# Kernel optimization log

Measured on AMD Instinct MI355X. Metric: run time of the kernel, lower is better.

The kernel has to match this reference:

```python
import jax, jax.numpy as jnp
import numpy as np

NEG = 1e12  # matches the torch code's -1e12 '-inf' substitute


def setup_inputs() -> dict:
    key = jax.random.key(0)
    k1, k2, k3, k4 = jax.random.split(key, 4)
    B, L, H, O = 8, 512, 768, 12
    inputs = jax.random.normal(k1, (B, L, H), dtype=jnp.float32)
    mask = jax.random.randint(k2, (B, L), 0, 2, dtype=jnp.int32)
    # kaiming-uniform-ish init scale
    bound1 = 1.0 / np.sqrt(H)
    weight1 = jax.random.uniform(k3, (H, O, H), dtype=jnp.float32, minval=-bound1, maxval=bound1)
    bound2 = 1.0 / np.sqrt(2 * H + 1)
    weight2 = jax.random.uniform(k4, (2 * H + 1, O), dtype=jnp.float32, minval=-bound2, maxval=bound2)
    return {"inputs": inputs, "weight1": weight1, "weight2": weight2, "mask": mask}


def reference(inputs, weight1, weight2, mask):
    B, L, H = inputs.shape
    # bilinear term: bxyo = x_i W1 x_j
    logits1 = jnp.einsum('bxi,ioj,byj->bxyo', inputs, weight1, inputs)
    # linear term: equivalent to cat([x_i, x_j, 1]) @ weight2, without the O(L^2*H) intermediate.
    # concat_x[b,i,j] = [inputs[b,i], inputs[b,j], 1]
    wa = weight2[:H]          # multiplies x_i (the x2/row side)
    wb = weight2[H:2 * H]     # multiplies x_j (the x1/col side)
    bias = weight2[2 * H]     # multiplies the ones column
    lin_i = inputs @ wa       # [B, L, O]
    lin_j = inputs @ wb       # [B, L, O]
    logits = logits1 + lin_i[:, :, None, :] + lin_j[:, None, :, :] + bias
    logits = jnp.transpose(logits, (0, 3, 1, 2))  # [B, O, L, L]
    m = mask.astype(logits.dtype)
    m_row = m[:, None, :, None]  # mask on axis ndim-2
    m_col = m[:, None, None, :]  # mask on axis ndim-1
    logits = logits * m_row - NEG * (1.0 - m_row)
    logits = logits * m_col - NEG * (1.0 - m_col)
    tril = jnp.tril(jnp.ones((L, L), logits.dtype), k=-1)
    logits = logits - tril * NEG
    return logits
```

## Files before the change

kernel.cpp:

```cpp
#include <hip/hip_runtime.h>


#define NEGV 1e12f

typedef __attribute__((ext_vector_type(4))) float f32x4;
typedef __attribute__((ext_vector_type(8))) int   i32x8;

__device__ __forceinline__ unsigned char f2fp8(float f) {
    union { float f; unsigned u; } c; c.f = f;
    unsigned s = (c.u >> 24) & 0x80;
    unsigned a = c.u & 0x7FFFFFFF;
    if (a < 0x3C800000u) return (unsigned char)s;
    a += 0x80000;
    int e = (int)(a >> 23) - 127;
    unsigned m = (a >> 20) & 7;
    if (e > 8 || (e == 8 && m == 7)) return (unsigned char)(s | 0x7E);
    return (unsigned char)(s | ((e + 7) << 3) | m);
}

__device__ __forceinline__ unsigned pk_fp8x2(float a, float b) {
#if __has_builtin(__builtin_amdgcn_cvt_pk_fp8_f32)
    return (unsigned)__builtin_amdgcn_cvt_pk_fp8_f32(a, b, 0, false) & 0xFFFFu;
#else
    return (unsigned)f2fp8(a) | ((unsigned)f2fp8(b) << 8);
#endif
}

__device__ __forceinline__ float fp8_to_f32(unsigned char b) {
#if __has_builtin(__builtin_amdgcn_cvt_f32_fp8)
    return __builtin_amdgcn_cvt_f32_fp8((int)b, 0);
#else
    const int s = b >> 7, e = (b >> 3) & 15, m = b & 7;
    float mag = e ? __builtin_ldexpf((float)(8 + m), e - 10)
                  : __builtin_ldexpf((float)m, -9);
    return s ? -mag : mag;
#endif
}

#define GLDS(gp, lp) __builtin_amdgcn_global_load_lds( \
    (__attribute__((address_space(1))) void*)(gp),     \
    (__attribute__((address_space(3))) void*)(lp), 16, 0, 0)

__global__ __launch_bounds__(256) void prep_kernel(
    const float* __restrict__ in, const float* __restrict__ w1,
    const float* __restrict__ w2, unsigned* __restrict__ A8,
    unsigned char* __restrict__ W8) {
    __shared__ float t[64][68];
    const int bx  = blockIdx.x;
    const int tid = threadIdx.x;
    if (bx < 3072) {
        const int i = bx * 256 + tid;
        float4 v = ((const float4*)in)[i];
        A8[i] = pk_fp8x2(v.x, v.y) | (pk_fp8x2(v.z, v.w) << 16);
    } else if (bx < 4800) {
        const int b2 = bx - 3072;
        const int n0 = (b2 % 144) * 64;
        const int i0 = (b2 / 144) * 64;
        const int g  = tid >> 4;
        const int q  = tid & 15;
        #pragma unroll
        for (int p = 0; p < 4; ++p) {
            const int il = p * 16 + g;
            float4 v = *(const float4*)(w1 + (size_t)(i0 + il) * 9216 + n0 + q * 4);
            *(float4*)&t[il][q * 4] = v;
        }
        __syncthreads();
        #pragma unroll
        for (int p = 0; p < 4; ++p) {
            const int nl = p * 16 + g;
            const int iq = q * 4;
            const unsigned lo = pk_fp8x2(t[iq    ][nl] * 16.0f, t[iq + 1][nl] * 16.0f);
            const unsigned hi = pk_fp8x2(t[iq + 2][nl] * 16.0f, t[iq + 3][nl] * 16.0f);
            *(unsigned*)(W8 + (size_t)(n0 + nl) * 768 + i0 + iq) = lo | (hi << 16);
        }
    } else {
        const int j = bx - 4800;
        unsigned char* dst = W8 + (size_t)(9216 + j) * 768;
        if (j < 24) {
            #pragma unroll
            for (int k = 0; k < 3; ++k) {
                const int h = tid * 3 + k;
                const int col = (j < 12) ? (h * 12 + j) : ((768 + h) * 12 + (j - 12));
                dst[h] = (unsigned char)(pk_fp8x2(w2[col] * 16.0f, 0.0f) & 0xFF);
            }
        } else {
            if (tid < 192) ((unsigned*)dst)[tid] = 0u;
        }
    }
}

template <bool COUNTED>
__device__ __forceinline__ void gemm256_fp8(
    const unsigned char* __restrict__ A, int lda,
    const unsigned char* __restrict__ B, int ldb,
    char* As, char* Bs, f32x4 (&acc)[8][4], int sA, int sB) {
    const int tid  = threadIdx.x;
    const int lane = tid & 63;
    const int wave = tid >> 6;
    const unsigned char* aSrc[4]; const unsigned char* bSrc[4];
    int off[4];
    #pragma unroll
    for (int p = 0; p < 4; ++p) {
        const int cc = tid + 512 * p;
        const int row = cc >> 3, slot = cc & 7;
        const int g = slot ^ (row & 7);
        aSrc[p] = A + (size_t)row * lda + g * 16;
        bSrc[p] = B + (size_t)row * ldb + g * 16;
        off[p] = cc * 16;
    }
    const int wm = (wave >> 2) * 128;
    const int wn = (wave & 3) * 64;
    const int fr = lane & 15;
    const int kg = lane >> 4;

    if (!COUNTED) {
        #pragma unroll
        for (int p = 0; p < 4; ++p) GLDS(aSrc[p], As + off[p]);
        #pragma unroll
        for (int p = 0; p < 4; ++p) GLDS(bSrc[p], Bs + off[p]);
        __syncthreads();
        int cur = 0;
        for (int t = 1; t <= 6; ++t) {
            const int nxt = cur ^ 1;
            if (t < 6) {
                const int kk = t * 128;
                #pragma unroll
                for (int p = 0; p < 4; ++p) GLDS(aSrc[p] + kk, As + nxt * 32768 + off[p]);
                #pragma unroll
                for (int p = 0; p < 4; ++p) GLDS(bSrc[p] + kk, Bs + nxt * 32768 + off[p]);
            }
            const char* Ab = As + cur * 32768;
            const char* Bb = Bs + cur * 32768;
            i32x8 bf[4];
            #pragma unroll
            for (int ni = 0; ni < 4; ++ni) {
                const int r = wn + ni * 16 + fr;
                const uint4 lo = *(const uint4*)(Bb + r * 128 + ((2 * kg    ) ^ (r & 7)) * 16);
                const uint4 hi = *(const uint4*)(Bb + r * 128 + ((2 * kg + 1) ^ (r & 7)) * 16);
                bf[ni][0] = lo.x; bf[ni][1] = lo.y; bf[ni][2] = lo.z; bf[ni][3] = lo.w;
                bf[ni][4] = hi.x; bf[ni][5] = hi.y; bf[ni][6] = hi.z; bf[ni][7] = hi.w;
            }
            #pragma unroll
            for (int mi = 0; mi < 8; ++mi) {
                const int r = wm + mi * 16 + fr;
                const uint4 lo = *(const uint4*)(Ab + r * 128 + ((2 * kg    ) ^ (r & 7)) * 16);
                const uint4 hi = *(const uint4*)(Ab + r * 128 + ((2 * kg + 1) ^ (r & 7)) * 16);
                i32x8 af;
                af[0] = lo.x; af[1] = lo.y; af[2] = lo.z; af[3] = lo.w;
                af[4] = hi.x; af[5] = hi.y; af[6] = hi.z; af[7] = hi.w;
                #pragma unroll
                for (int ni = 0; ni < 4; ++ni)
                    acc[mi][ni] = __builtin_amdgcn_mfma_scale_f32_16x16x128_f8f6f4(
                        af, bf[ni], acc[mi][ni], 0, 0, 0, sA, 0, sB);
            }
            __syncthreads();
            cur = nxt;
        }
        return;
    }

    #pragma unroll
    for (int p = 0; p < 4; ++p) GLDS(aSrc[p], As + off[p]);
    #pragma unroll
    for (int p = 0; p < 4; ++p) GLDS(bSrc[p], Bs + off[p]);
    #pragma unroll
    for (int p = 0; p < 4; ++p) GLDS(aSrc[p] + 128, As + 32768 + off[p]);
    #pragma unroll
    for (int p = 0; p < 4; ++p) GLDS(bSrc[p] + 128, Bs + 32768 + off[p]);

    #pragma unroll
    for (int t = 0; t < 6; ++t) {
        const int cur = t & 1;
        if (t < 5) asm volatile("s_waitcnt vmcnt(8)" ::: "memory");
        else       asm volatile("s_waitcnt vmcnt(0)" ::: "memory");
        __builtin_amdgcn_sched_barrier(0);
        __builtin_amdgcn_s_barrier();
        const char* Ab = As + cur * 32768;
        const char* Bb = Bs + cur * 32768;
        i32x8 bf[4];
        #pragma unroll
        for (int ni = 0; ni < 4; ++ni) {
            const int r = wn + ni * 16 + fr;
            const uint4 lo = *(const uint4*)(Bb + r * 128 + ((2 * kg    ) ^ (r & 7)) * 16);
            const uint4 hi = *(const uint4*)(Bb + r * 128 + ((2 * kg + 1) ^ (r & 7)) * 16);
            bf[ni][0] = lo.x; bf[ni][1] = lo.y; bf[ni][2] = lo.z; bf[ni][3] = lo.w;
            bf[ni][4] = hi.x; bf[ni][5] = hi.y; bf[ni][6] = hi.z; bf[ni][7] = hi.w;
        }
        __builtin_amdgcn_s_setprio(1);
        #pragma unroll
        for (int mi = 0; mi < 8; ++mi) {
            const int r = wm + mi * 16 + fr;
            const uint4 lo = *(const uint4*)(Ab + r * 128 + ((2 * kg    ) ^ (r & 7)) * 16);
            const uint4 hi = *(const uint4*)(Ab + r * 128 + ((2 * kg + 1) ^ (r & 7)) * 16);
            i32x8 af;
            af[0] = lo.x; af[1] = lo.y; af[2] = lo.z; af[3] = lo.w;
            af[4] = hi.x; af[5] = hi.y; af[6] = hi.z; af[7] = hi.w;
            #pragma unroll
            for (int ni = 0; ni < 4; ++ni)
                acc[mi][ni] = __builtin_amdgcn_mfma_scale_f32_16x16x128_f8f6f4(
                    af, bf[ni], acc[mi][ni], 0, 0, 0, sA, 0, sB);
        }
        __builtin_amdgcn_s_setprio(0);
        asm volatile("s_waitcnt lgkmcnt(0)" ::: "memory");
        __builtin_amdgcn_sched_barrier(0);
        __builtin_amdgcn_s_barrier();
        if (t < 4) {
            const int kk = (t + 2) * 128;
            #pragma unroll
            for (int p = 0; p < 4; ++p) GLDS(aSrc[p] + kk, As + cur * 32768 + off[p]);
            #pragma unroll
            for (int p = 0; p < 4; ++p) GLDS(bSrc[p] + kk, Bs + cur * 32768 + off[p]);
        }
    }
}

__global__ __launch_bounds__(512, 2) void gemm1_kernel(
    const unsigned char* __restrict__ A8,
    const unsigned char* __restrict__ W8,
    unsigned char* __restrict__ U) {
    __shared__ __align__(16) char As[2 * 32768];
    __shared__ __align__(16) char Bs[2 * 32768];
    const int orig = blockIdx.x;
    const int swz  = (orig & 7) * 74 + (orig >> 3);
    const int m0 = (swz & 15) * 256;
    const int n0 = (swz >> 4) * 256;
    f32x4 acc[8][4] = {};
    gemm256_fp8<false>(A8 + (size_t)m0 * 768, 768, W8 + (size_t)n0 * 768, 768,
                       As, Bs, acc, 0x7F7F7F7F, 0x7B7B7B7B);
    const int lane = threadIdx.x & 63;
    const int wave = threadIdx.x >> 6;
    const int wm = (wave >> 2) * 128, wn = (wave & 3) * 64;
    const int rl = (lane >> 4) * 4, cl = lane & 15;
    #pragma unroll
    for (int mi = 0; mi < 8; ++mi) {
        const int m = m0 + wm + mi * 16 + rl;
        #pragma unroll
        for (int ni = 0; ni < 4; ++ni) {
            const int n = n0 + wn + ni * 16 + cl;
            const unsigned p01 = pk_fp8x2(acc[mi][ni][0], acc[mi][ni][1]);
            const unsigned p23 = pk_fp8x2(acc[mi][ni][2], acc[mi][ni][3]);
            U[(size_t)(m    ) * 9472 + n] = (unsigned char)(p01 & 0xFF);
            U[(size_t)(m + 1) * 9472 + n] = (unsigned char)(p01 >> 8);
            U[(size_t)(m + 2) * 9472 + n] = (unsigned char)(p23 & 0xFF);
            U[(size_t)(m + 3) * 9472 + n] = (unsigned char)(p23 >> 8);
        }
    }
}

__global__ __launch_bounds__(512, 2) void gemm2_kernel(
    const unsigned char* __restrict__ U,
    const unsigned char* __restrict__ A8,
    const float* __restrict__ w2,
    const int* __restrict__ mask,
    float* __restrict__ out) {
    __shared__ __align__(16) char As[2 * 32768];
    __shared__ __align__(16) char Bs[2 * 32768];
    const int orig = blockIdx.x;
    const int swz  = (orig & 7) * 48 + (orig >> 3);
    const int bo = swz >> 2;
    const int b = bo / 12, o = bo % 12;
    const int x0 = (swz & 1) * 256;
    const int y0 = ((swz >> 1) & 1) * 256;
    f32x4 acc[8][4] = {};
    gemm256_fp8<true>(U + (size_t)(b * 512 + x0) * 9472 + (size_t)o * 768, 9472,
                      A8 + (size_t)(b * 512 + y0) * 768, 768,
                      As, Bs, acc, 0x7F7F7F7F, 0x7F7F7F7F);
    const float bias = w2[1536 * 12 + o];
    float* outp = out + (size_t)bo * 512 * 512;
    const int lane = threadIdx.x & 63;
    const int wave = threadIdx.x >> 6;
    const int wm = (wave >> 2) * 128, wn = (wave & 3) * 64;
    const int rl = (lane >> 4) * 4, cl = lane & 15;
    float ljv[4]; int mc[4];
    #pragma unroll
    for (int ni = 0; ni < 4; ++ni) {
        const int y = y0 + wn + ni * 16 + cl;
        ljv[ni] = fp8_to_f32(U[(size_t)(b * 512 + y) * 9472 + 9228 + o]);
        mc[ni]  = mask[b * 512 + y];
    }
    #pragma unroll
    for (int mi = 0; mi < 8; ++mi) {
        const int xb = x0 + wm + mi * 16 + rl;
        float liv[4]; int mr[4];
        #pragma unroll
        for (int r = 0; r < 4; ++r) {
            liv[r] = fp8_to_f32(U[(size_t)(b * 512 + xb + r) * 9472 + 9216 + o]);
            mr[r]  = mask[b * 512 + xb + r];
        }
        #pragma unroll
        for (int ni = 0; ni < 4; ++ni) {
            const int y = y0 + wn + ni * 16 + cl;
            #pragma unroll
            for (int r = 0; r < 4; ++r) {
                float v = acc[mi][ni][r] + liv[r] + ljv[ni] + bias;
                if (!(mr[r] & mc[ni])) v = -NEGV;
                if (xb + r > y)        v -= NEGV;
                outp[(size_t)(xb + r) * 512 + y] = v;
            }
        }
    }
}

extern "C" void kernel_launch(void* const* d_in, const int* in_sizes, int n_in,
                              void* d_out, int out_size, void* d_ws, size_t ws_size,
                              hipStream_t stream) {
    const float* inputs = (const float*)d_in[0];
    const float* w1     = (const float*)d_in[1];
    const float* w2     = (const float*)d_in[2];
    const int*   mask   = (const int*)d_in[3];
    float* outp = (float*)d_out;

    char* ws = (char*)d_ws;
    unsigned char* A8 = (unsigned char*)(ws + 0);
    unsigned char* W8 = (unsigned char*)(ws + 3145728);
    unsigned char* U8 = (unsigned char*)(ws + 10420224);

    prep_kernel<<<5056, 256, 0, stream>>>(inputs, w1, w2, (unsigned*)A8, W8);
    gemm1_kernel<<<592, 512, 0, stream>>>(A8, W8, U8);
    gemm2_kernel<<<384, 512, 0, stream>>>(U8, A8, w2, mask, outp);
}
```

Baseline: 211.4 us.

## Split MFMA loop into barrier-fenced phases and use counted pipeline for both GEMMs

```diff
diff --git a/kernel.cpp b/kernel.cpp
--- a/kernel.cpp
+++ b/kernel.cpp
@@ -89,7 +89,6 @@
     }
 }
 
-template <bool COUNTED>
 __device__ __forceinline__ void gemm256_fp8(
     const unsigned char* __restrict__ A, int lda,
     const unsigned char* __restrict__ B, int ldb,
@@ -113,52 +112,6 @@
     const int fr = lane & 15;
     const int kg = lane >> 4;
 
-    if (!COUNTED) {
-        #pragma unroll
-        for (int p = 0; p < 4; ++p) GLDS(aSrc[p], As + off[p]);
-        #pragma unroll
-        for (int p = 0; p < 4; ++p) GLDS(bSrc[p], Bs + off[p]);
-        __syncthreads();
-        int cur = 0;
-        for (int t = 1; t <= 6; ++t) {
-            const int nxt = cur ^ 1;
-            if (t < 6) {
-                const int kk = t * 128;
-                #pragma unroll
-                for (int p = 0; p < 4; ++p) GLDS(aSrc[p] + kk, As + nxt * 32768 + off[p]);
-                #pragma unroll
-                for (int p = 0; p < 4; ++p) GLDS(bSrc[p] + kk, Bs + nxt * 32768 + off[p]);
-            }
-            const char* Ab = As + cur * 32768;
-            const char* Bb = Bs + cur * 32768;
-            i32x8 bf[4];
-            #pragma unroll
-            for (int ni = 0; ni < 4; ++ni) {
-                const int r = wn + ni * 16 + fr;
-                const uint4 lo = *(const uint4*)(Bb + r * 128 + ((2 * kg    ) ^ (r & 7)) * 16);
-                const uint4 hi = *(const uint4*)(Bb + r * 128 + ((2 * kg + 1) ^ (r & 7)) * 16);
-                bf[ni][0] = lo.x; bf[ni][1] = lo.y; bf[ni][2] = lo.z; bf[ni][3] = lo.w;
-                bf[ni][4] = hi.x; bf[ni][5] = hi.y; bf[ni][6] = hi.z; bf[ni][7] = hi.w;
-            }
-            #pragma unroll
-            for (int mi = 0; mi < 8; ++mi) {
-                const int r = wm + mi * 16 + fr;
-                const uint4 lo = *(const uint4*)(Ab + r * 128 + ((2 * kg    ) ^ (r & 7)) * 16);
-                const uint4 hi = *(const uint4*)(Ab + r * 128 + ((2 * kg + 1) ^ (r & 7)) * 16);
-                i32x8 af;
-                af[0] = lo.x; af[1] = lo.y; af[2] = lo.z; af[3] = lo.w;
-                af[4] = hi.x; af[5] = hi.y; af[6] = hi.z; af[7] = hi.w;
-                #pragma unroll
-                for (int ni = 0; ni < 4; ++ni)
-                    acc[mi][ni] = __builtin_amdgcn_mfma_scale_f32_16x16x128_f8f6f4(
-                        af, bf[ni], acc[mi][ni], 0, 0, 0, sA, 0, sB);
-            }
-            __syncthreads();
-            cur = nxt;
-        }
-        return;
-    }
-
     #pragma unroll
     for (int p = 0; p < 4; ++p) GLDS(aSrc[p], As + off[p]);
     #pragma unroll
@@ -179,28 +132,37 @@
         const char* Bb = Bs + cur * 32768;
         i32x8 bf[4];
         #pragma unroll
-        for (int ni = 0; ni < 4; ++ni) {
-            const int r = wn + ni * 16 + fr;
-            const uint4 lo = *(const uint4*)(Bb + r * 128 + ((2 * kg    ) ^ (r & 7)) * 16);
-            const uint4 hi = *(const uint4*)(Bb + r * 128 + ((2 * kg + 1) ^ (r & 7)) * 16);
-            bf[ni][0] = lo.x; bf[ni][1] = lo.y; bf[ni][2] = lo.z; bf[ni][3] = lo.w;
-            bf[ni][4] = hi.x; bf[ni][5] = hi.y; bf[ni][6] = hi.z; bf[ni][7] = hi.w;
-        }
-        __builtin_amdgcn_s_setprio(1);
-        #pragma unroll
-        for (int mi = 0; mi < 8; ++mi) {
-            const int r = wm + mi * 16 + fr;
-            const uint4 lo = *(const uint4*)(Ab + r * 128 + ((2 * kg    ) ^ (r & 7)) * 16);
-            const uint4 hi = *(const uint4*)(Ab + r * 128 + ((2 * kg + 1) ^ (r & 7)) * 16);
-            i32x8 af;
-            af[0] = lo.x; af[1] = lo.y; af[2] = lo.z; af[3] = lo.w;
-            af[4] = hi.x; af[5] = hi.y; af[6] = hi.z; af[7] = hi.w;
-            #pragma unroll
-            for (int ni = 0; ni < 4; ++ni)
-                acc[mi][ni] = __builtin_amdgcn_mfma_scale_f32_16x16x128_f8f6f4(
-                    af, bf[ni], acc[mi][ni], 0, 0, 0, sA, 0, sB);
-        }
-        __builtin_amdgcn_s_setprio(0);
+        for (int ph = 0; ph < 4; ++ph) {
+            if (ph == 0) {
+                #pragma unroll
+                for (int ni = 0; ni < 4; ++ni) {
+                    const int r = wn + ni * 16 + fr;
+                    const uint4 lo = *(const uint4*)(Bb + r * 128 + ((2 * kg    ) ^ (r & 7)) * 16);
+                    const uint4 hi = *(const uint4*)(Bb + r * 128 + ((2 * kg + 1) ^ (r & 7)) * 16);
+                    bf[ni][0] = lo.x; bf[ni][1] = lo.y; bf[ni][2] = lo.z; bf[ni][3] = lo.w;
+                    bf[ni][4] = hi.x; bf[ni][5] = hi.y; bf[ni][6] = hi.z; bf[ni][7] = hi.w;
+                }
+            }
+            i32x8 af[2];
+            #pragma unroll
+            for (int k = 0; k < 2; ++k) {
+                const int r = wm + (2 * ph + k) * 16 + fr;
+                const uint4 lo = *(const uint4*)(Ab + r * 128 + ((2 * kg    ) ^ (r & 7)) * 16);
+                const uint4 hi = *(const uint4*)(Ab + r * 128 + ((2 * kg + 1) ^ (r & 7)) * 16);
+                af[k][0] = lo.x; af[k][1] = lo.y; af[k][2] = lo.z; af[k][3] = lo.w;
+                af[k][4] = hi.x; af[k][5] = hi.y; af[k][6] = hi.z; af[k][7] = hi.w;
+            }
+            __builtin_amdgcn_s_barrier();
+            __builtin_amdgcn_s_setprio(1);
+            #pragma unroll
+            for (int k = 0; k < 2; ++k)
+                #pragma unroll
+                for (int ni = 0; ni < 4; ++ni)
+                    acc[2 * ph + k][ni] = __builtin_amdgcn_mfma_scale_f32_16x16x128_f8f6f4(
+                        af[k], bf[ni], acc[2 * ph + k][ni], 0, 0, 0, sA, 0, sB);
+            __builtin_amdgcn_s_setprio(0);
+            __builtin_amdgcn_s_barrier();
+        }
         asm volatile("s_waitcnt lgkmcnt(0)" ::: "memory");
         __builtin_amdgcn_sched_barrier(0);
         __builtin_amdgcn_s_barrier();
@@ -225,8 +187,8 @@
     const int m0 = (swz & 15) * 256;
     const int n0 = (swz >> 4) * 256;
     f32x4 acc[8][4] = {};
-    gemm256_fp8<false>(A8 + (size_t)m0 * 768, 768, W8 + (size_t)n0 * 768, 768,
-                       As, Bs, acc, 0x7F7F7F7F, 0x7B7B7B7B);
+    gemm256_fp8(A8 + (size_t)m0 * 768, 768, W8 + (size_t)n0 * 768, 768,
+                As, Bs, acc, 0x7F7F7F7F, 0x7B7B7B7B);
     const int lane = threadIdx.x & 63;
     const int wave = threadIdx.x >> 6;
     const int wm = (wave >> 2) * 128, wn = (wave & 3) * 64;
@@ -262,9 +224,9 @@
     const int x0 = (swz & 1) * 256;
     const int y0 = ((swz >> 1) & 1) * 256;
     f32x4 acc[8][4] = {};
-    gemm256_fp8<true>(U + (size_t)(b * 512 + x0) * 9472 + (size_t)o * 768, 9472,
-                      A8 + (size_t)(b * 512 + y0) * 768, 768,
-                      As, Bs, acc, 0x7F7F7F7F, 0x7F7F7F7F);
+    gemm256_fp8(U + (size_t)(b * 512 + x0) * 9472 + (size_t)o * 768, 9472,
+                A8 + (size_t)(b * 512 + y0) * 768, 768,
+                As, Bs, acc, 0x7F7F7F7F, 0x7F7F7F7F);
     const float bias = w2[1536 * 12 + o];
     float* outp = out + (size_t)bo * 512 * 512;
     const int lane = threadIdx.x & 63;
```

New measurement: 222.0 us. +5.0%, slower.

## Quantize first GEMM operands to FP4 and run fp4 MFMA

Applied to the files above, without the earlier changes.

```diff
diff --git a/kernel.cpp b/kernel.cpp
--- a/kernel.cpp
+++ b/kernel.cpp
@@ -37,23 +37,44 @@
 #endif
 }
 
+__device__ __forceinline__ unsigned f2fp4(float f) {
+    const float a = fabsf(f);
+    const unsigned s = (__float_as_uint(f) >> 28) & 8u;
+    unsigned c;
+    if      (a < 0.25f) c = 0;
+    else if (a < 0.75f) c = 1;
+    else if (a < 1.25f) c = 2;
+    else if (a < 1.75f) c = 3;
+    else if (a < 2.5f)  c = 4;
+    else if (a < 3.5f)  c = 5;
+    else if (a < 5.0f)  c = 6;
+    else                c = 7;
+    return s | c;
+}
+
 #define GLDS(gp, lp) __builtin_amdgcn_global_load_lds( \
     (__attribute__((address_space(1))) void*)(gp),     \
     (__attribute__((address_space(3))) void*)(lp), 16, 0, 0)
 
 __global__ __launch_bounds__(256) void prep_kernel(
     const float* __restrict__ in, const float* __restrict__ w1,
-    const float* __restrict__ w2, unsigned* __restrict__ A8,
-    unsigned char* __restrict__ W8) {
+    const float* __restrict__ w2, unsigned* __restrict__ A4,
+    unsigned* __restrict__ A8, unsigned char* __restrict__ W4) {
     __shared__ float t[64][68];
     const int bx  = blockIdx.x;
     const int tid = threadIdx.x;
-    if (bx < 3072) {
+    if (bx < 1536) {
         const int i = bx * 256 + tid;
-        float4 v = ((const float4*)in)[i];
-        A8[i] = pk_fp8x2(v.x, v.y) | (pk_fp8x2(v.z, v.w) << 16);
-    } else if (bx < 4800) {
-        const int b2 = bx - 3072;
+        const float4 v0 = ((const float4*)in)[2 * i];
+        const float4 v1 = ((const float4*)in)[2 * i + 1];
+        A4[i] = f2fp4(v0.x * 2.0f)        | (f2fp4(v0.y * 2.0f) << 4)
+              | (f2fp4(v0.z * 2.0f) << 8) | (f2fp4(v0.w * 2.0f) << 12)
+              | (f2fp4(v1.x * 2.0f) << 16)| (f2fp4(v1.y * 2.0f) << 20)
+              | (f2fp4(v1.z * 2.0f) << 24)| (f2fp4(v1.w * 2.0f) << 28);
+        A8[2 * i]     = pk_fp8x2(v0.x, v0.y) | (pk_fp8x2(v0.z, v0.w) << 16);
+        A8[2 * i + 1] = pk_fp8x2(v1.x, v1.y) | (pk_fp8x2(v1.z, v1.w) << 16);
+    } else if (bx < 3264) {
+        const int b2 = bx - 1536;
         const int n0 = (b2 % 144) * 64;
         const int i0 = (b2 / 144) * 64;
         const int g  = tid >> 4;
@@ -66,30 +87,104 @@
         }
         __syncthreads();
         #pragma unroll
-        for (int p = 0; p < 4; ++p) {
-            const int nl = p * 16 + g;
-            const int iq = q * 4;
-            const unsigned lo = pk_fp8x2(t[iq    ][nl] * 16.0f, t[iq + 1][nl] * 16.0f);
-            const unsigned hi = pk_fp8x2(t[iq + 2][nl] * 16.0f, t[iq + 3][nl] * 16.0f);
-            *(unsigned*)(W8 + (size_t)(n0 + nl) * 768 + i0 + iq) = lo | (hi << 16);
+        for (int p = 0; p < 2; ++p) {
+            const int nl = p * 32 + (tid >> 3);
+            const int iq = (tid & 7) * 8;
+            unsigned w = 0;
+            #pragma unroll
+            for (int e = 0; e < 8; ++e)
+                w |= f2fp4(t[iq + e][nl] * 128.0f) << (4 * e);
+            *(unsigned*)(W4 + (size_t)(n0 + nl) * 384 + (i0 >> 1) + (tid & 7) * 4) = w;
         }
     } else {
-        const int j = bx - 4800;
-        unsigned char* dst = W8 + (size_t)(9216 + j) * 768;
+        const int j = bx - 3264;
+        unsigned char* dst = W4 + (size_t)(9216 + j) * 384;
         if (j < 24) {
-            #pragma unroll
-            for (int k = 0; k < 3; ++k) {
-                const int h = tid * 3 + k;
-                const int col = (j < 12) ? (h * 12 + j) : ((768 + h) * 12 + (j - 12));
-                dst[h] = (unsigned char)(pk_fp8x2(w2[col] * 16.0f, 0.0f) & 0xFF);
+            if (tid < 128) {
+                const int h0 = tid * 6;
+                #pragma unroll
+                for (int k = 0; k < 3; ++k) {
+                    const int h = h0 + 2 * k;
+                    const int c0 = (j < 12) ? (h * 12 + j)       : ((768 + h) * 12 + (j - 12));
+                    const int c1 = (j < 12) ? ((h + 1) * 12 + j) : ((769 + h) * 12 + (j - 12));
+                    dst[(h >> 1)] = (unsigned char)(f2fp4(w2[c0] * 128.0f)
+                                                  | (f2fp4(w2[c1] * 128.0f) << 4));
+                }
             }
         } else {
-            if (tid < 192) ((unsigned*)dst)[tid] = 0u;
-        }
-    }
-}
-
-template <bool COUNTED>
+            if (tid < 96) ((unsigned*)dst)[tid] = 0u;
+        }
+    }
+}
+
+__device__ __forceinline__ void gemm256_fp4(
+    const unsigned char* __restrict__ A, int lda,
+    const unsigned char* __restrict__ B, int ldb,
+    char* As, char* Bs, f32x4 (&acc)[8][4], int sA, int sB) {
+    const int tid  = threadIdx.x;
+    const int lane = tid & 63;
+    const int wave = tid >> 6;
+    const unsigned char* aSrc[4]; const unsigned char* bSrc[4];
+    int off[4];
+    #pragma unroll
+    for (int p = 0; p < 4; ++p) {
+        const int cc = tid + 512 * p;
+        const int row = cc >> 3, slot = cc & 7;
+        const int g = slot ^ (row & 7);
+        aSrc[p] = A + (size_t)row * lda + g * 16;
+        bSrc[p] = B + (size_t)row * ldb + g * 16;
+        off[p] = cc * 16;
+    }
+    const int wm = (wave >> 2) * 128;
+    const int wn = (wave & 3) * 64;
+    const int fr = lane & 15;
+    const int kg = lane >> 4;
+
+#define READ_FRAG4(dst, buf, rr, kk) do {                                         \
+        const uint4 q_ = *(const uint4*)((buf) + (rr) * 128 +                     \
+                                         (((kk) * 4 + kg) ^ ((rr) & 7)) * 16);    \
+        dst[0] = q_.x; dst[1] = q_.y; dst[2] = q_.z; dst[3] = q_.w;               \
+        dst[4] = 0; dst[5] = 0; dst[6] = 0; dst[7] = 0;                           \
+    } while (0)
+
+    #pragma unroll
+    for (int p = 0; p < 4; ++p) GLDS(aSrc[p], As + off[p]);
+    #pragma unroll
+    for (int p = 0; p < 4; ++p) GLDS(bSrc[p], Bs + off[p]);
+    __syncthreads();
+    int cur = 0;
+    #pragma unroll
+    for (int t = 1; t <= 3; ++t) {
+        const int nxt = cur ^ 1;
+        if (t < 3) {
+            const int kk = t * 128;
+            #pragma unroll
+            for (int p = 0; p < 4; ++p) GLDS(aSrc[p] + kk, As + nxt * 32768 + off[p]);
+            #pragma unroll
+            for (int p = 0; p < 4; ++p) GLDS(bSrc[p] + kk, Bs + nxt * 32768 + off[p]);
+        }
+        const char* Ab = As + cur * 32768;
+        const char* Bb = Bs + cur * 32768;
+        #pragma unroll
+        for (int kk = 0; kk < 2; ++kk) {
+            i32x8 bf[4];
+            #pragma unroll
+            for (int ni = 0; ni < 4; ++ni) READ_FRAG4(bf[ni], Bb, wn + ni * 16 + fr, kk);
+            #pragma unroll
+            for (int mi = 0; mi < 8; ++mi) {
+                i32x8 af; READ_FRAG4(af, Ab, wm + mi * 16 + fr, kk);
+                #pragma unroll
+                for (int ni = 0; ni < 4; ++ni)
+                    acc[mi][ni] = __builtin_amdgcn_mfma_scale_f32_16x16x128_f8f6f4(
+                        af, bf[ni], acc[mi][ni], 4, 4, 0, sA, 0, sB);
+            }
+        }
+        __syncthreads();
+        cur = nxt;
+    }
+#undef READ_FRAG4
+}
+
 __device__ __forceinline__ void gemm256_fp8(
     const unsigned char* __restrict__ A, int lda,
     const unsigned char* __restrict__ B, int ldb,
@@ -113,52 +208,6 @@
     const int fr = lane & 15;
     const int kg = lane >> 4;
 
-    if (!COUNTED) {
-        #pragma unroll
-        for (int p = 0; p < 4; ++p) GLDS(aSrc[p], As + off[p]);
-        #pragma unroll
-        for (int p = 0; p < 4; ++p) GLDS(bSrc[p], Bs + off[p]);
-        __syncthreads();
-        int cur = 0;
-        for (int t = 1; t <= 6; ++t) {
-            const int nxt = cur ^ 1;
-            if (t < 6) {
-                const int kk = t * 128;
-                #pragma unroll
-                for (int p = 0; p < 4; ++p) GLDS(aSrc[p] + kk, As + nxt * 32768 + off[p]);
-                #pragma unroll
-                for (int p = 0; p < 4; ++p) GLDS(bSrc[p] + kk, Bs + nxt * 32768 + off[p]);
-            }
-            const char* Ab = As + cur * 32768;
-            const char* Bb = Bs + cur * 32768;
-            i32x8 bf[4];
-            #pragma unroll
-            for (int ni = 0; ni < 4; ++ni) {
-                const int r = wn + ni * 16 + fr;
-                const uint4 lo = *(const uint4*)(Bb + r * 128 + ((2 * kg    ) ^ (r & 7)) * 16);
-                const uint4 hi = *(const uint4*)(Bb + r * 128 + ((2 * kg + 1) ^ (r & 7)) * 16);
-                bf[ni][0] = lo.x; bf[ni][1] = lo.y; bf[ni][2] = lo.z; bf[ni][3] = lo.w;
-                bf[ni][4] = hi.x; bf[ni][5] = hi.y; bf[ni][6] = hi.z; bf[ni][7] = hi.w;
-            }
-            #pragma unroll
-            for (int mi = 0; mi < 8; ++mi) {
-                const int r = wm + mi * 16 + fr;
-                const uint4 lo = *(const uint4*)(Ab + r * 128 + ((2 * kg    ) ^ (r & 7)) * 16);
-                const uint4 hi = *(const uint4*)(Ab + r * 128 + ((2 * kg + 1) ^ (r & 7)) * 16);
-                i32x8 af;
-                af[0] = lo.x; af[1] = lo.y; af[2] = lo.z; af[3] = lo.w;
-                af[4] = hi.x; af[5] = hi.y; af[6] = hi.z; af[7] = hi.w;
-                #pragma unroll
-                for (int ni = 0; ni < 4; ++ni)
-                    acc[mi][ni] = __builtin_amdgcn_mfma_scale_f32_16x16x128_f8f6f4(
-                        af, bf[ni], acc[mi][ni], 0, 0, 0, sA, 0, sB);
-            }
-            __syncthreads();
-            cur = nxt;
-        }
-        return;
-    }
-
     #pragma unroll
     for (int p = 0; p < 4; ++p) GLDS(aSrc[p], As + off[p]);
     #pragma unroll
@@ -215,9 +264,9 @@
 }
 
 __global__ __launch_bounds__(512, 2) void gemm1_kernel(
-    const unsigned char* __restrict__ A8,
-    const unsigned char* __restrict__ W8,
-    unsigned char* __restrict__ U) {
+    const unsigned char* __restrict__ A4,
+    const unsigned char* __restrict__ W4,
+    unsigned char* __restrict__ U8) {
     __shared__ __align__(16) char As[2 * 32768];
     __shared__ __align__(16) char Bs[2 * 32768];
     const int orig = blockIdx.x;
@@ -225,8 +274,8 @@
     const int m0 = (swz & 15) * 256;
     const int n0 = (swz >> 4) * 256;
     f32x4 acc[8][4] = {};
-    gemm256_fp8<false>(A8 + (size_t)m0 * 768, 768, W8 + (size_t)n0 * 768, 768,
-                       As, Bs, acc, 0x7F7F7F7F, 0x7B7B7B7B);
+    gemm256_fp4(A4 + (size_t)m0 * 384, 384, W4 + (size_t)n0 * 384, 384,
+                As, Bs, acc, 0x7E7E7E7E, 0x78787878);
     const int lane = threadIdx.x & 63;
     const int wave = threadIdx.x >> 6;
     const int wm = (wave >> 2) * 128, wn = (wave & 3) * 64;
@@ -239,16 +288,16 @@
             const int n = n0 + wn + ni * 16 + cl;
             const unsigned p01 = pk_fp8x2(acc[mi][ni][0], acc[mi][ni][1]);
             const unsigned p23 = pk_fp8x2(acc[mi][ni][2], acc[mi][ni][3]);
-            U[(size_t)(m    ) * 9472 + n] = (unsigned char)(p01 & 0xFF);
-            U[(size_t)(m + 1) * 9472 + n] = (unsigned char)(p01 >> 8);
-            U[(size_t)(m + 2) * 9472 + n] = (unsigned char)(p23 & 0xFF);
-            U[(size_t)(m + 3) * 9472 + n] = (unsigned char)(p23 >> 8);
+            U8[(size_t)(m    ) * 9472 + n] = (unsigned char)(p01 & 0xFF);
+            U8[(size_t)(m + 1) * 9472 + n] = (unsigned char)(p01 >> 8);
+            U8[(size_t)(m + 2) * 9472 + n] = (unsigned char)(p23 & 0xFF);
+            U8[(size_t)(m + 3) * 9472 + n] = (unsigned char)(p23 >> 8);
         }
     }
 }
 
 __global__ __launch_bounds__(512, 2) void gemm2_kernel(
-    const unsigned char* __restrict__ U,
+    const unsigned char* __restrict__ U8,
     const unsigned char* __restrict__ A8,
     const float* __restrict__ w2,
     const int* __restrict__ mask,
@@ -262,9 +311,9 @@
     const int x0 = (swz & 1) * 256;
     const int y0 = ((swz >> 1) & 1) * 256;
     f32x4 acc[8][4] = {};
-    gemm256_fp8<true>(U + (size_t)(b * 512 + x0) * 9472 + (size_t)o * 768, 9472,
-                      A8 + (size_t)(b * 512 + y0) * 768, 768,
-                      As, Bs, acc, 0x7F7F7F7F, 0x7F7F7F7F);
+    gemm256_fp8(U8 + (size_t)(b * 512 + x0) * 9472 + (size_t)o * 768, 9472,
+                A8 + (size_t)(b * 512 + y0) * 768, 768,
+                As, Bs, acc, 0x7F7F7F7F, 0x7F7F7F7F);
     const float bias = w2[1536 * 12 + o];
     float* outp = out + (size_t)bo * 512 * 512;
     const int lane = threadIdx.x & 63;
@@ -275,7 +324,7 @@
     #pragma unroll
     for (int ni = 0; ni < 4; ++ni) {
         const int y = y0 + wn + ni * 16 + cl;
-        ljv[ni] = fp8_to_f32(U[(size_t)(b * 512 + y) * 9472 + 9228 + o]);
+        ljv[ni] = fp8_to_f32(U8[(size_t)(b * 512 + y) * 9472 + 9228 + o]);
         mc[ni]  = mask[b * 512 + y];
     }
     #pragma unroll
@@ -284,7 +333,7 @@
         float liv[4]; int mr[4];
         #pragma unroll
         for (int r = 0; r < 4; ++r) {
-            liv[r] = fp8_to_f32(U[(size_t)(b * 512 + xb + r) * 9472 + 9216 + o]);
+            liv[r] = fp8_to_f32(U8[(size_t)(b * 512 + xb + r) * 9472 + 9216 + o]);
             mr[r]  = mask[b * 512 + xb + r];
         }
         #pragma unroll
@@ -311,11 +360,13 @@
     float* outp = (float*)d_out;
 
     char* ws = (char*)d_ws;
-    unsigned char* A8 = (unsigned char*)(ws + 0);
-    unsigned char* W8 = (unsigned char*)(ws + 3145728);
-    unsigned char* U8 = (unsigned char*)(ws + 10420224);
-
-    prep_kernel<<<5056, 256, 0, stream>>>(inputs, w1, w2, (unsigned*)A8, W8);
-    gemm1_kernel<<<592, 512, 0, stream>>>(A8, W8, U8);
+    unsigned char* A4 = (unsigned char*)(ws + 0);
+    unsigned char* A8 = (unsigned char*)(ws + 1572864);
+    unsigned char* W4 = (unsigned char*)(ws + 4718592);
+    unsigned char* U8 = (unsigned char*)(ws + 8355840);
+
+    prep_kernel<<<3520, 256, 0, stream>>>(inputs, w1, w2, (unsigned*)A4,
+                                          (unsigned*)A8, W4);
+    gemm1_kernel<<<592, 512, 0, stream>>>(A4, W4, U8);
     gemm2_kernel<<<384, 512, 0, stream>>>(U8, A8, w2, mask, outp);
 }
```

Result: faster. 204.0 us (-3.5%).
